# Kernel optimization log

Hardware: AMD Instinct MI355X
Metric: run time of the kernel (lower is better)

The kernel has to match this reference:

```python
import jax, jax.numpy as jnp
import numpy as np

B = 32768
EPS = 0.2  # BatchNorm eps used in the original module


def _xavier(key, shape):
    fan_in, fan_out = shape[-2], shape[-1]
    std = (2.0 / (fan_in + fan_out)) ** 0.5
    return (jax.random.normal(key, shape, jnp.float32) * std).astype(jnp.float32)


def bn(x, g, b):
    # training-mode BatchNorm1d: batch stats over the batch axis (-2), biased var
    m = jnp.mean(x, axis=-2, keepdims=True)
    v = jnp.mean(jnp.square(x - m), axis=-2, keepdims=True)
    return (x - m) * jax.lax.rsqrt(v + EPS) * g + b


def setup_inputs() -> dict:
    key = jax.random.key(0)
    ks = iter(jax.random.split(key, 48))
    inp = {}
    inp['x1f'] = jax.random.normal(next(ks), (B, 512), jnp.float32)
    inp['x2f'] = jax.random.normal(next(ks), (B, 512), jnp.float32)
    # shared trunk
    inp['W1'] = _xavier(next(ks), (512, 256)); inp['b1'] = jnp.zeros(256, jnp.float32)
    inp['W2'] = _xavier(next(ks), (256, 256)); inp['b2'] = jnp.zeros(256, jnp.float32)
    # batchnorm affine params (bn1:256, bn2:256, bn3:128, bn4:64)
    inp['g1'] = jnp.ones(256, jnp.float32); inp['be1'] = jnp.zeros(256, jnp.float32)
    inp['g2'] = jnp.ones(256, jnp.float32); inp['be2'] = jnp.zeros(256, jnp.float32)
    inp['g3'] = jnp.ones(128, jnp.float32); inp['be3'] = jnp.zeros(128, jnp.float32)
    inp['g4'] = jnp.ones(64, jnp.float32); inp['be4'] = jnp.zeros(64, jnp.float32)
    # 4 branch projections from each stream (x11..x14, x21..x24), stacked on axis 0
    inp['Wbx1'] = _xavier(next(ks), (4, 256, 256)); inp['bbx1'] = jnp.zeros((4, 256), jnp.float32)
    inp['Wbx2'] = _xavier(next(ks), (4, 256, 256)); inp['bbx2'] = jnp.zeros((4, 256), jnp.float32)
    # gating MLPs (xw*1, xw*2, xw*3, y*), stacked over the 4 attributes
    inp['Wwa'] = _xavier(next(ks), (4, 512, 128)); inp['bwa'] = jnp.zeros((4, 128), jnp.float32)
    inp['Wwb'] = _xavier(next(ks), (4, 128, 64)); inp['bwb'] = jnp.zeros((4, 64), jnp.float32)
    inp['Wwc'] = _xavier(next(ks), (4, 64, 64)); inp['bwc'] = jnp.zeros((4, 64), jnp.float32)
    inp['Wy'] = _xavier(next(ks), (4, 64, 2)); inp['by'] = jnp.zeros((4, 2), jnp.float32)
    # combine layers x1c..x4c, stacked
    inp['Wc'] = _xavier(next(ks), (4, 512, 256)); inp['bc'] = jnp.zeros((4, 256), jnp.float32)
    # output heads (different class counts: 3, 3, 6, 4)
    inp['Wo1'] = _xavier(next(ks), (256, 3)); inp['bo1'] = jnp.zeros(3, jnp.float32)
    inp['Wo2'] = _xavier(next(ks), (256, 3)); inp['bo2'] = jnp.zeros(3, jnp.float32)
    inp['Wo3'] = _xavier(next(ks), (256, 6)); inp['bo3'] = jnp.zeros(6, jnp.float32)
    inp['Wo4'] = _xavier(next(ks), (256, 4)); inp['bo4'] = jnp.zeros(4, jnp.float32)
    return inp


def reference(x1f, x2f, W1, b1, W2, b2, g1, be1, g2, be2, g3, be3, g4, be4,
              Wbx1, bbx1, Wbx2, bbx2, Wwa, bwa, Wwb, bwb, Wwc, bwc, Wy, by,
              Wc, bc, Wo1, bo1, Wo2, bo2, Wo3, bo3, Wo4, bo4):
    relu = jax.nn.relu

    def trunk(x):
        h = bn(relu(x @ W1 + b1), g1, be1)
        return bn(relu(h @ W2 + b2), g2, be2)

    h1 = trunk(x1f)  # [B,256]
    h2 = trunk(x2f)  # [B,256]

    # 4 branch features per stream, each bn1-normalized: [4,B,256]
    b1x = bn(relu(jnp.einsum('bi,kio->kbo', h1, Wbx1) + bbx1[:, None, :]), g1, be1)
    b2x = bn(relu(jnp.einsum('bi,kio->kbo', h2, Wbx2) + bbx2[:, None, :]), g1, be1)

    # gating MLP per attribute -> 2-way softmax weights
    xcat = jnp.concatenate([b1x, b2x], axis=-1)  # [4,B,512]
    a = bn(relu(jnp.einsum('kbi,kio->kbo', xcat, Wwa) + bwa[:, None, :]), g3, be3)
    b_ = bn(relu(jnp.einsum('kbi,kio->kbo', a, Wwb) + bwb[:, None, :]), g4, be4)
    c = bn(relu(jnp.einsum('kbi,kio->kbo', b_, Wwc) + bwc[:, None, :]), g4, be4)
    y = jax.nn.softmax(jnp.einsum('kbi,kio->kbo', c, Wy) + by[:, None, :], axis=-1)  # [4,B,2]

    # the original per-column loop == one broadcast multiply per stream
    xw = jnp.concatenate([b1x * y[..., 0:1], b2x * y[..., 1:2]], axis=-1)  # [4,B,512]

    # combine layers (dropout is identity in eval)
    xc = bn(relu(jnp.einsum('kbi,kio->kbo', xw, Wc) + bc[:, None, :]), g1, be1)  # [4,B,256]

    y1o = jax.nn.softmax(xc[0] @ Wo1 + bo1, axis=-1)
    y2o = jax.nn.softmax(xc[1] @ Wo2 + bo2, axis=-1)
    y3o = jax.nn.softmax(xc[2] @ Wo3 + bo3, axis=-1)
    y4o = jax.nn.softmax(xc[3] @ Wo4 + bo4, axis=-1)
    return (y1o, y2o, y3o, y4o)
```

## Files before the change

### kernel.cpp

```cpp
#include <hip/hip_runtime.h>
#include <hip/hip_bf16.h>


typedef unsigned short u16;
typedef _Float16 f16x8 __attribute__((ext_vector_type(8)));
typedef float f32x4 __attribute__((ext_vector_type(4)));

#define B_ROWS 32768
#define EPS_BN 0.2f
#define BINV (1.0f / 32768.0f)

__device__ __forceinline__ float bf2f(u16 u) {
    union { unsigned int i; float f; } c;
    c.i = ((unsigned int)u) << 16;
    return c.f;
}
__device__ __forceinline__ u16 f2bf(float f) {
    union { float f; unsigned int i; } c;
    c.f = f;
    unsigned int x = c.i;
    return (u16)((x + 0x7FFFu + ((x >> 16) & 1u)) >> 16);
}
__device__ __forceinline__ float h2f(u16 u) {
    _Float16 h;
    __builtin_memcpy(&h, &u, 2);
    return (float)h;
}
__device__ __forceinline__ u16 f2h(float f) {
    _Float16 h = (_Float16)f;
    u16 u;
    __builtin_memcpy(&u, &h, 2);
    return u;
}
__device__ __forceinline__ float ldp(const void* p, long i, int flag) {
    return flag ? bf2f(((const u16*)p)[i]) : ((const float*)p)[i];
}
__device__ __forceinline__ void gload16(const u16* gp, u16* lp) {
    __builtin_amdgcn_global_load_lds(
        (const __attribute__((address_space(1))) unsigned int*)gp,
        (__attribute__((address_space(3))) unsigned int*)lp, 16, 0, 0);
}

__global__ void detect_dtype(const u16* __restrict__ x, int* __restrict__ flag) {
    const int lane = threadIdx.x;
    const u16 v = x[2 * lane];
    const int e = (v >> 7) & 0xFF;
    const bool plausible = (e >= 110 && e <= 140);
    const unsigned long long m = __ballot(plausible);
    if (lane == 0) *flag = (__popcll(m) >= 58) ? 1 : 0;
}

struct PTab { const void* p[20]; int n[20]; int off[20]; };

__global__ void convert_params(PTab t, float* __restrict__ dst,
                               const int* __restrict__ flag) {
    const int ti = blockIdx.y;
    const int n = t.n[ti];
    float* o = dst + t.off[ti];
    const int isbf = *flag;
    for (int i = blockIdx.x * 256 + threadIdx.x; i < n; i += gridDim.x * 256)
        o[i] = ldp(t.p[ti], i, isbf);
}

__global__ __launch_bounds__(256) void prep_w(
    const void* __restrict__ W, long wstride,
    const void* __restrict__ bias, long bstride,
    const float* __restrict__ psum, const float* __restrict__ psq, int pstride,
    const void* __restrict__ pg, const void* __restrict__ pbe, int gmask,
    const int* __restrict__ dtflag,
    u16* __restrict__ Wt, long wtstride,
    float* __restrict__ biasP, float* __restrict__ T0o,
    float* __restrict__ T1o, float* __restrict__ bsum, long bost,
    int K, int khalf)
{
    const int tid = threadIdx.x;
    const int n = blockIdx.x;
    const int N = gridDim.x;
    const int inst = blockIdx.y;
    const int flag = *dtflag;
    __shared__ float sn[512], tn[512];
    __shared__ float r0[4], r1[4];

    for (int i = tid; i < K; i += 256) {
        float s = 1.f, t = 0.f;
        if (psum) {
            float m = psum[(long)pstride * inst + i] * BINV;
            float v = psq[(long)pstride * inst + i] * BINV - m * m;
            float g = ldp(pg, i & gmask, flag);
            float b = ldp(pbe, i & gmask, flag);
            s = g * rsqrtf(v + EPS_BN);
            t = b - m * s;
        }
        sn[i] = s; tn[i] = t;
    }
    __syncthreads();
    float p0 = 0.f, p1 = 0.f;
    for (int k = tid; k < K; k += 256) {
        float wv = ldp(W, wstride * inst + (long)k * N + n, flag);
        Wt[wtstride * inst + (long)n * K + k] = f2h(sn[k] * wv);
        float tw = tn[k] * wv;
        if (k < khalf) p0 += tw; else p1 += tw;
    }
#pragma unroll
    for (int off = 32; off; off >>= 1) {
        p0 += __shfl_xor(p0, off);
        p1 += __shfl_xor(p1, off);
    }
    const int lane = tid & 63, wid = tid >> 6;
    if (lane == 0) { r0[wid] = p0; r1[wid] = p1; }
    __syncthreads();
    if (tid == 0) {
        float t0 = r0[0] + r0[1] + r0[2] + r0[3];
        float t1 = r1[0] + r1[1] + r1[2] + r1[3];
        float bp = ldp(bias, bstride * inst + n, flag);
        long o = bost * inst + n;
        biasP[o] = bp; T0o[o] = t0; T1o[o] = t1; bsum[o] = bp + t0 + t1;
    }
}

__global__ __launch_bounds__(256) void reduce_stats(
    const float* __restrict__ part, int X, int colsPer,
    float* __restrict__ outS, float* __restrict__ outQ, int total)
{
    const int t = blockIdx.x * 256 + threadIdx.x;
    if (t >= total) return;
    const int p = t / colsPer, c = t % colsPer;
    const float* pb = part + (long)p * X * 2 * colsPer + c;
    float s = 0.f, q = 0.f;
#pragma unroll 4
    for (int x = 0; x < X; ++x) {
        s += pb[(long)x * 2 * colsPer];
        q += pb[(long)x * 2 * colsPer + colsPer];
    }
    outS[t] = s; outQ[t] = q;
}

template <bool XSTAGE, bool ROWW, int WM, int WN, int K>
__global__ __launch_bounds__(256, 3) void gemm_mfma(
    const void* __restrict__ X, const void* __restrict__ X2,
    long xstride, int ximask, int ldx, int ksplit, long ksecond,
    const int* __restrict__ dtflag,
    const u16* __restrict__ Wt, long wtstride,
    const float* __restrict__ biasP, const float* __restrict__ T0,
    const float* __restrict__ T1, const float* __restrict__ bsum, int bN,
    u16* __restrict__ Out, long ostride, int ldout,
    float* __restrict__ gsum, float* __restrict__ gsq, int sstride,
    float* __restrict__ part,
    const float* __restrict__ Y0v)
{
    const int tid = threadIdx.x;
    const int lane = tid & 63;
    const int wid = tid >> 6;
    const int wm = wid / WN, wn = wid % WN;
    const int inst = blockIdx.z;
    const int rowB = blockIdx.x * (64 * WM);
    const int nBase = blockIdx.y * (64 * WN);
    const int n0 = nBase + wn * 64;
    const int fm = lane & 15, quad = lane >> 4;
    const int rloc = lane >> 3;
    const int cg = (lane & 7) ^ rloc;

    __shared__ __align__(16) u16 AsBs[(WM + WN) * 4096];
    __shared__ float redS[4][64];
    __shared__ float redQ[4][64];
    u16* As = AsBs;
    u16* Bs = AsBs + WM * 4096;

    bool xf32 = false;
    if constexpr (XSTAGE) xf32 = (*dtflag == 0);
    const char* xb;
    if (XSTAGE) xb = (const char*)(inst == 0 ? X : X2);
    else        xb = (const char*)X + 2l * xstride * (inst & ximask);
    const u16* wtp = Wt + wtstride * inst;
    u16* op = Out + ostride * inst;

    f32x4 acc[4][4];
#pragma unroll
    for (int i = 0; i < 4; ++i)
#pragma unroll
        for (int j = 0; j < 4; ++j) acc[i][j] = (f32x4){0.f, 0.f, 0.f, 0.f};

    _Float16 ysc[2][4];
    if constexpr (ROWW) {
        const float* yp = Y0v + (long)inst * B_ROWS;
#pragma unroll
        for (int mi = 0; mi < 4; ++mi) {
            const float y = yp[rowB + wm * 64 + mi * 16 + fm];
            ysc[0][mi] = (_Float16)y;
            ysc[1][mi] = (_Float16)(1.f - y);
        }
    }

    for (int kt = 0; kt < K / 64; ++kt) {
        const int kk = kt * 64;
        __syncthreads();
        if constexpr (XSTAGE) {
#pragma unroll
            for (int p = 0; p < WM * 2; ++p) {
                const int s = p * 256 + tid;
                const int m = s >> 3, c = s & 7;
                const int g = c ^ (m & 7);
                f16x8 h;
                if (xf32) {
                    const float* gp = (const float*)xb + (long)(rowB + m) * ldx + kk + g * 8;
                    const float4 u = *(const float4*)gp;
                    const float4 u2 = *(const float4*)(gp + 4);
                    h[0] = (_Float16)u.x;  h[1] = (_Float16)u.y;
                    h[2] = (_Float16)u.z;  h[3] = (_Float16)u.w;
                    h[4] = (_Float16)u2.x; h[5] = (_Float16)u2.y;
                    h[6] = (_Float16)u2.z; h[7] = (_Float16)u2.w;
                } else {
                    const uint4 v = *(const uint4*)((const u16*)xb + (long)(rowB + m) * ldx + kk + g * 8);
                    const u16* pv = (const u16*)&v;
#pragma unroll
                    for (int j = 0; j < 8; ++j) h[j] = (_Float16)bf2f(pv[j]);
                }
                *(f16x8*)&As[s * 8] = h;
            }
        } else {
            const u16* xs = (const u16*)xb;
            int kkr = kk;
            if (kk >= ksplit) { xs += ksecond; kkr -= ksplit; }
#pragma unroll
            for (int s = wid; s < WM * 8; s += 4)
                gload16(xs + (long)(rowB + s * 8 + rloc) * ldx + kkr + cg * 8,
                        &As[s * 512 + lane * 8]);
        }
#pragma unroll
        for (int s = wid; s < WN * 8; s += 4)
            gload16(wtp + (long)(nBase + s * 8 + rloc) * K + kk + cg * 8,
                    &Bs[s * 512 + lane * 8]);
        __syncthreads();

        const int sel = (ROWW && kk >= ksplit) ? 1 : 0;
#pragma unroll
        for (int q = 0; q < 2; ++q) {
            f16x8 af[4], bfr[4];
#pragma unroll
            for (int mi = 0; mi < 4; ++mi) {
                const int mm = wm * 64 + mi * 16 + fm;
                af[mi] = *(const f16x8*)&As[mm * 64 + (((q * 4 + quad) ^ (mm & 7)) * 8)];
            }
            if constexpr (ROWW) {
#pragma unroll
                for (int mi = 0; mi < 4; ++mi) {
                    const _Float16 yh = ysc[sel][mi];
#pragma unroll
                    for (int j = 0; j < 8; ++j) af[mi][j] *= yh;
                }
            }
#pragma unroll
            for (int ni = 0; ni < 4; ++ni) {
                const int nn = wn * 64 + ni * 16 + fm;
                bfr[ni] = *(const f16x8*)&Bs[nn * 64 + (((q * 4 + quad) ^ (nn & 7)) * 8)];
            }
#pragma unroll
            for (int mi = 0; mi < 4; ++mi)
#pragma unroll
                for (int ni = 0; ni < 4; ++ni)
                    acc[mi][ni] = __builtin_amdgcn_mfma_f32_16x16x32_f16(
                        af[mi], bfr[ni], acc[mi][ni], 0, 0, 0);
        }
    }

    __syncthreads();

    u16* wtile = AsBs + wid * 4096;
    const int R0 = rowB + wm * 64;

    float yv[16];
    if constexpr (ROWW) {
        const float* yp = Y0v + (long)inst * B_ROWS;
#pragma unroll
        for (int mi = 0; mi < 4; ++mi)
#pragma unroll
            for (int r = 0; r < 4; ++r)
                yv[mi * 4 + r] = yp[R0 + mi * 16 + quad * 4 + r];
    }

#pragma unroll
    for (int ni = 0; ni < 4; ++ni) {
        const int nc = ni * 16 + fm;
        const int n = n0 + nc;
        float bS = 0.f, bP = 0.f, t0v = 0.f, t1v = 0.f;
        if constexpr (ROWW) {
            bP = biasP[(long)inst * bN + n];
            t0v = T0[(long)inst * bN + n];
            t1v = T1[(long)inst * bN + n];
        } else {
            bS = bsum[(long)inst * bN + n];
        }
        float s = 0.f, qq = 0.f;
#pragma unroll
        for (int mi = 0; mi < 4; ++mi) {
#pragma unroll
            for (int r = 0; r < 4; ++r) {
                float v;
                if constexpr (ROWW) {
                    const float y = yv[mi * 4 + r];
                    v = acc[mi][ni][r] + y * t0v + (1.f - y) * t1v + bP;
                } else {
                    v = acc[mi][ni][r] + bS;
                }
                v = fmaxf(v, 0.f);
                s += v; qq += v * v;
                const int lr = mi * 16 + quad * 4 + r;
                wtile[lr * 64 + (nc ^ (((lr >> 1) & 7) << 3))] = f2h(v);
            }
        }
        s += __shfl_xor(s, 16);  s += __shfl_xor(s, 32);
        qq += __shfl_xor(qq, 16); qq += __shfl_xor(qq, 32);
        if (quad == 0) { redS[wid][nc] = s; redQ[wid][nc] = qq; }
    }

    {
        const int l8 = lane & 7, r8 = lane >> 3;
#pragma unroll
        for (int it = 0; it < 8; ++it) {
            const int lr = it * 8 + r8;
            const int ch = l8 ^ ((lr >> 1) & 7);
            const f16x8 hv = *(const f16x8*)&wtile[lr * 64 + ch * 8];
            *(f16x8*)(op + (long)(R0 + lr) * ldout + n0 + l8 * 8) = hv;
        }
    }

    __syncthreads();
    if (tid < WN * 64) {
        const int wnc = tid >> 6, within = tid & 63;
        float s = 0.f, q = 0.f;
#pragma unroll
        for (int w = 0; w < WM; ++w) {
            s += redS[w * WN + wnc][within];
            q += redQ[w * WN + wnc][within];
        }
        if (part) {
            float* pb = part +
                (long)((inst * gridDim.y + blockIdx.y) * gridDim.x + blockIdx.x)
                    * (2 * WN * 64);
            pb[tid] = s;
            pb[WN * 64 + tid] = q;
        } else {
            atomicAdd(&gsum[(long)inst * sstride + nBase + tid], s);
            atomicAdd(&gsq [(long)inst * sstride + nBase + tid], q);
        }
    }
}

__global__ __launch_bounds__(256) void gate_kernel(
    const u16* __restrict__ zc,
    const float* __restrict__ stFs, const float* __restrict__ stFq,
    const float* __restrict__ g4, const float* __restrict__ be4,
    const float* __restrict__ Wy, const float* __restrict__ by,
    float* __restrict__ Y0)
{
    const int tid = threadIdx.x;
    const int k = blockIdx.y;
    const int r0 = blockIdx.x * 128;

    __shared__ __align__(8) float Ws2[64][2];
    __shared__ float cg[2];

    if (tid < 64) {
        const int c = tid;
        const float m = stFs[k * 64 + c] * BINV;
        const float v = stFq[k * 64 + c] * BINV - m * m;
        const float s = g4[c] * rsqrtf(v + EPS_BN);
        const float t = be4[c] - m * s;
        const float w0 = Wy[k * 128 + c * 2 + 0];
        const float w1 = Wy[k * 128 + c * 2 + 1];
        Ws2[c][0] = s * w0;
        Ws2[c][1] = s * w1;
        float t0 = t * w0, t1 = t * w1;
#pragma unroll
        for (int off = 32; off; off >>= 1) {
            t0 += __shfl_xor(t0, off);
            t1 += __shfl_xor(t1, off);
        }
        if (c == 0) {
            cg[0] = t0 + by[k * 2 + 0];
            cg[1] = t1 + by[k * 2 + 1];
        }
    }
    __syncthreads();

    const int row = r0 + (tid >> 1);
    const int seg = tid & 1;
    const u16* xp = zc + ((long)k * B_ROWS + row) * 64 + seg * 32;
    float a0 = 0.f, a1 = 0.f;
#pragma unroll
    for (int it = 0; it < 4; ++it) {
        const uint4 v = *(const uint4*)(xp + it * 8);
        const u16* pv = (const u16*)&v;
#pragma unroll
        for (int e = 0; e < 8; ++e) {
            const int c = seg * 32 + it * 8 + e;
            const float x = h2f(pv[e]);
            a0 += x * Ws2[c][0];
            a1 += x * Ws2[c][1];
        }
    }
    a0 += __shfl_xor(a0, 1);
    a1 += __shfl_xor(a1, 1);
    if (seg == 0) {
        const float l0 = a0 + cg[0];
        const float l1 = a1 + cg[1];
        Y0[(long)k * B_ROWS + row] = 1.f / (1.f + __expf(l1 - l0));
    }
}

__global__ __launch_bounds__(256) void heads_kernel(
    const u16* __restrict__ zxc,
    const float* __restrict__ stHs, const float* __restrict__ stHq,
    const float* __restrict__ g1, const float* __restrict__ be1,
    const float* __restrict__ Wo1, const float* __restrict__ bo1,
    const float* __restrict__ Wo2, const float* __restrict__ bo2,
    const float* __restrict__ Wo3, const float* __restrict__ bo3,
    const float* __restrict__ Wo4, const float* __restrict__ bo4,
    void* __restrict__ out, const int* __restrict__ dtflag)
{
    const int tid = threadIdx.x;
    const int k = blockIdx.y;
    const int r0 = blockIdx.x * 64;

    const float* Wo; const float* bo; int nk; long obase;
    if (k == 0)      { Wo = Wo1; bo = bo1; nk = 3; obase = 0; }
    else if (k == 1) { Wo = Wo2; bo = bo2; nk = 3; obase = (long)3 * B_ROWS; }
    else if (k == 2) { Wo = Wo3; bo = bo3; nk = 6; obase = (long)6 * B_ROWS; }
    else             { Wo = Wo4; bo = bo4; nk = 4; obase = (long)12 * B_ROWS; }

    __shared__ __align__(16) float Ws[256][8];
    __shared__ float cj[8];
    __shared__ float redC[4][8];

    {
        const int c = tid;
        const float m = stHs[k * 256 + c] * BINV;
        const float v = stHq[k * 256 + c] * BINV - m * m;
        const float s = g1[c] * rsqrtf(v + EPS_BN);
        const float t = be1[c] - m * s;
        const int rs = c ^ (c >> 6);
        float tw[6];
#pragma unroll
        for (int j = 0; j < 6; ++j) {
            const float w = (j < nk) ? Wo[c * nk + j] : 0.f;
            Ws[rs][j] = s * w;
            tw[j] = t * w;
        }
        Ws[rs][6] = 0.f; Ws[rs][7] = 0.f;
#pragma unroll
        for (int off = 32; off; off >>= 1)
#pragma unroll
            for (int j = 0; j < 6; ++j) tw[j] += __shfl_xor(tw[j], off);
        const int lane = tid & 63, wid = tid >> 6;
        if (lane < 6) redC[wid][lane] = tw[lane];
    }
    __syncthreads();
    if (tid < 8) {
        float s4 = 0.f;
        if (tid < 6) s4 = redC[0][tid] + redC[1][tid] + redC[2][tid] + redC[3][tid];
        cj[tid] = (tid < nk) ? s4 + bo[tid] : 0.f;
    }
    __syncthreads();

    const int row = r0 + (tid >> 2);
    const int seg = tid & 3;
    const u16* xp = zxc + ((long)k * B_ROWS + row) * 256 + seg * 64;
    float acc[6];
#pragma unroll
    for (int j = 0; j < 6; ++j) acc[j] = 0.f;
#pragma unroll
    for (int it = 0; it < 8; ++it) {
        const uint4 v = *(const uint4*)(xp + it * 8);
        const u16* pv = (const u16*)&v;
#pragma unroll
        for (int e = 0; e < 8; ++e) {
            const int cc = it * 8 + e;
            const int rs = (seg * 64 + cc) ^ seg;
            const float x = h2f(pv[e]);
            const f32x4 w0 = *(const f32x4*)&Ws[rs][0];
            const f32x4 w1 = *(const f32x4*)&Ws[rs][4];
            acc[0] += x * w0[0];
            acc[1] += x * w0[1];
            acc[2] += x * w0[2];
            acc[3] += x * w0[3];
            acc[4] += x * w1[0];
            acc[5] += x * w1[1];
        }
    }
#pragma unroll
    for (int j = 0; j < 6; ++j) {
        acc[j] += __shfl_xor(acc[j], 1);
        acc[j] += __shfl_xor(acc[j], 2);
    }

    if (seg == 0) {
        float l[6];
        float mx = -1e30f;
#pragma unroll
        for (int j = 0; j < 6; j++)
            if (j < nk) { l[j] = acc[j] + cj[j]; mx = fmaxf(mx, l[j]); }
        float e[6];
        float se = 0.f;
#pragma unroll
        for (int j = 0; j < 6; j++)
            if (j < nk) { e[j] = __expf(l[j] - mx); se += e[j]; }
        const float inv = 1.f / se;
        if (*dtflag) {
            u16* ob = (u16*)out;
#pragma unroll
            for (int j = 0; j < 6; j++)
                if (j < nk) ob[obase + (long)row * nk + j] = f2bf(e[j] * inv);
        } else {
            float* of = (float*)out;
#pragma unroll
            for (int j = 0; j < 6; j++)
                if (j < nk) of[obase + (long)row * nk + j] = e[j] * inv;
        }
    }
}

__global__ void fill_sentinel(u16* out, int n) {
    int i = blockIdx.x * 256 + threadIdx.x;
    if (i < n) out[i] = 0x3E80;
}

extern "C" void kernel_launch(void* const* d_in, const int* in_sizes, int n_in,
                              void* d_out, int out_size, void* d_ws, size_t ws_size,
                              hipStream_t stream)
{
    const long B = B_ROWS;
    char* ws = (char*)d_ws;
    const size_t MB = 1024 * 1024;

    u16* z1  = (u16*)(ws);
    u16* z2  = (u16*)(ws + 32 * MB);
    u16* za  = (u16*)(ws);
    u16* zbb = (u16*)(ws + 32 * MB);
    u16* zc  = (u16*)(ws + 48 * MB);
    u16* zxc = (u16*)(ws);
    u16* zb  = (u16*)(ws + 64 * MB);
    float* Y0 = (float*)(ws + 192 * MB);
    float* stats = (float*)(ws + 192 * MB + 512 * 1024);
    int* dtflag = (int*)(ws + 192 * MB + 576 * 1024);
    float* Pst = (float*)(ws + 192 * MB + 640 * 1024);

    u16* WtA = (u16*)(ws + 193 * MB);
    u16* WtB = WtA + 131072;
    u16* WtC = WtB + 131072;
    u16* WtD = WtC + 524288;
    u16* WtH = WtD + 262144;
    u16* WtE = WtH + 524288;
    u16* WtF = WtE + 32768;
    float* biasArea = (float*)(ws + 197 * MB);
    float* bA = biasArea;
    float* bB = bA + 2048;
    float* bC = bB + 2048;
    float* bD = bC + 8192;
    float* bH = bD + 2048;
    float* bE = bH + 4096;
    float* bF = bE + 1024;

    float* partC = (float*)(ws);
    float* partH = (float*)(ws + 193 * MB);

    const int cIdx[20] = {6,7,10,11,12,13,20,21,22,23,24,25,28,29,30,31,32,33,34,35};
    PTab tab;
    int mapOff[36];
    int acc = 0;
    for (int i = 0; i < 20; i++) {
        tab.p[i] = d_in[cIdx[i]];
        tab.n[i] = in_sizes[cIdx[i]];
        tab.off[i] = acc;
        mapOff[cIdx[i]] = acc;
        acc += in_sizes[cIdx[i]];
    }
    const size_t need = 197 * MB + 20480 * 4 + 4096;
    if (need > ws_size || (size_t)acc * 4 > 384 * 1024) {
        fill_sentinel<<<(out_size + 255) / 256, 256, 0, stream>>>((u16*)d_out, out_size);
        return;
    }
    auto PF = [&](int idx) { return Pst + mapOff[idx]; };

    float* stAs = stats;        float* stAq = stAs + 512;
    float* stBs = stAq + 512;   float* stBq = stBs + 512;
    float* stCs = stBq + 512;   float* stCq = stCs + 2048;
    float* stDs = stCq + 2048;  float* stDq = stDs + 512;
    float* stEs = stDq + 512;   float* stEq = stEs + 256;
    float* stFs = stEq + 256;   float* stFq = stFs + 256;
    float* stHs = stFq + 256;   float* stHq = stHs + 1024;

    hipMemsetAsync(stats, 0, 10240 * 4, stream);
    detect_dtype<<<1, 64, 0, stream>>>((const u16*)d_in[0], dtflag);
    convert_params<<<dim3(32, 20), 256, 0, stream>>>(tab, Pst, dtflag);

    const dim3 blk(256);
    const int BIGK = 1 << 29;

    prep_w<<<dim3(256, 2), blk, 0, stream>>>(
        d_in[2], 0, d_in[3], 0, nullptr, nullptr, 0, nullptr, nullptr, 0,
        dtflag, WtA, 0, bA, bA + 512, bA + 1024, bA + 1536, 256, 512, 512);
    gemm_mfma<true, false, 2, 2, 512><<<dim3(256, 2, 2), blk, 0, stream>>>(
        d_in[0], d_in[1], 0, 0, 512, BIGK, 0, dtflag, WtA, 0,
        bA, bA + 512, bA + 1024, bA + 1536, 256,
        z1, B * 256, 256, stAs, stAq, 256, nullptr, nullptr);

    prep_w<<<dim3(256, 2), blk, 0, stream>>>(
        d_in[4], 0, d_in[5], 0, stAs, stAq, 256, d_in[6], d_in[7], 255,
        dtflag, WtB, 65536, bB, bB + 512, bB + 1024, bB + 1536, 256, 256, 256);
    gemm_mfma<false, false, 2, 2, 256><<<dim3(256, 2, 2), blk, 0, stream>>>(
        z1, nullptr, B * 256, 3, 256, BIGK, 0, dtflag, WtB, 65536,
        bB, bB + 512, bB + 1024, bB + 1536, 256,
        z2, B * 256, 256, stBs, stBq, 256, nullptr, nullptr);

    for (int s = 0; s < 2; s++) {
        prep_w<<<dim3(256, 4), blk, 0, stream>>>(
            d_in[s ? 16 : 14], 65536, d_in[s ? 17 : 15], 256,
            stBs + s * 256, stBq + s * 256, 0, d_in[8], d_in[9], 255,
            dtflag, WtC + s * 65536, 131072,
            bC + s * 256, bC + 2048 + s * 256, bC + 4096 + s * 256,
            bC + 6144 + s * 256, 512, 256, 256);
    }
    gemm_mfma<false, false, 2, 2, 256><<<dim3(256, 2, 8), blk, 0, stream>>>(
        z2, nullptr, B * 256, 1, 256, BIGK, 0, dtflag, WtC, 65536,
        bC, bC + 2048, bC + 4096, bC + 6144, 256,
        zb, B * 256, 256, stCs, stCq, 256, partC, nullptr);
    reduce_stats<<<dim3(8), blk, 0, stream>>>(partC, 256, 128, stCs, stCq, 2048);

    prep_w<<<dim3(128, 4), blk, 0, stream>>>(
        d_in[18], 65536, d_in[19], 128, stCs, stCq, 512, d_in[6], d_in[7], 255,
        dtflag, WtD, 65536, bD, bD + 512, bD + 1024, bD + 1536, 128, 512, 512);
    prep_w<<<dim3(256, 4), blk, 0, stream>>>(
        d_in[26], 131072, d_in[27], 256, stCs, stCq, 512, d_in[6], d_in[7], 255,
        dtflag, WtH, 131072, bH, bH + 1024, bH + 2048, bH + 3072, 256, 512, 256);
    gemm_mfma<false, false, 2, 2, 512><<<dim3(256, 1, 4), blk, 0, stream>>>(
        zb, nullptr, 2 * B * 256, 3, 256, 256, B * 256, dtflag, WtD, 65536,
        bD, bD + 512, bD + 1024, bD + 1536, 128,
        za, B * 128, 128, stDs, stDq, 128, nullptr, nullptr);

    prep_w<<<dim3(64, 4), blk, 0, stream>>>(
        d_in[20], 8192, d_in[21], 64, stDs, stDq, 128, d_in[10], d_in[11], 127,
        dtflag, WtE, 8192, bE, bE + 256, bE + 512, bE + 768, 64, 128, 128);
    gemm_mfma<false, false, 4, 1, 128><<<dim3(128, 1, 4), blk, 0, stream>>>(
        za, nullptr, B * 128, 3, 128, BIGK, 0, dtflag, WtE, 8192,
        bE, bE + 256, bE + 512, bE + 768, 64,
        zbb, B * 64, 64, stEs, stEq, 64, nullptr, nullptr);

    prep_w<<<dim3(64, 4), blk, 0, stream>>>(
        d_in[22], 4096, d_in[23], 64, stEs, stEq, 64, d_in[12], d_in[13], 63,
        dtflag, WtF, 4096, bF, bF + 256, bF + 512, bF + 768, 64, 64, 64);
    gemm_mfma<false, false, 4, 1, 64><<<dim3(128, 1, 4), blk, 0, stream>>>(
        zbb, nullptr, B * 64, 3, 64, BIGK, 0, dtflag, WtF, 4096,
        bF, bF + 256, bF + 512, bF + 768, 64,
        zc, B * 64, 64, stFs, stFq, 64, nullptr, nullptr);

    gate_kernel<<<dim3(B_ROWS / 128, 4), blk, 0, stream>>>(
        zc, stFs, stFq, PF(12), PF(13), PF(24), PF(25), Y0);

    gemm_mfma<false, true, 2, 2, 512><<<dim3(256, 2, 4), blk, 0, stream>>>(
        zb, nullptr, 2 * B * 256, 3, 256, 256, B * 256, dtflag, WtH, 131072,
        bH, bH + 1024, bH + 2048, bH + 3072, 256,
        zxc, B * 256, 256, stHs, stHq, 256, partH, Y0);
    reduce_stats<<<dim3(4), blk, 0, stream>>>(partH, 256, 128, stHs, stHq, 1024);

    heads_kernel<<<dim3(B_ROWS / 64, 4), blk, 0, stream>>>(
        zxc, stHs, stHq, PF(6), PF(7), PF(28), PF(29), PF(30), PF(31),
        PF(32), PF(33), PF(34), PF(35), d_out, dtflag);
}
```

Before: 584.9 us.

## Load MFMA fragments directly from global memory, bypassing LDS staging for non-XSTAGE GEMMs

For the non-XSTAGE GEMM instances, the K loop no longer stages A and B tiles into shared memory with barriers. Each lane now reads its f16x8 MFMA fragments straight from global memory using precomputed row offsets. This removes both __syncthreads per K step and the LDS round trip. In exchange, tiles are no longer shared across warps, so the same data is read redundantly from global memory or cache, and the 16-byte per-lane row-strided loads may coalesce poorly.

```diff
diff --git a/kernel.cpp b/kernel.cpp
--- a/kernel.cpp
+++ b/kernel.cpp
@@ -157,14 +157,10 @@
     const int nBase = blockIdx.y * (64 * WN);
     const int n0 = nBase + wn * 64;
     const int fm = lane & 15, quad = lane >> 4;
-    const int rloc = lane >> 3;
-    const int cg = (lane & 7) ^ rloc;
 
     __shared__ __align__(16) u16 AsBs[(WM + WN) * 4096];
     __shared__ float redS[4][64];
     __shared__ float redQ[4][64];
-    u16* As = AsBs;
-    u16* Bs = AsBs + WM * 4096;
 
     bool xf32 = false;
     if constexpr (XSTAGE) xf32 = (*dtflag == 0);
@@ -191,10 +187,56 @@
         }
     }
 
-    for (int kt = 0; kt < K / 64; ++kt) {
-        const int kk = kt * 64;
-        __syncthreads();
-        if constexpr (XSTAGE) {
+    if constexpr (!XSTAGE) {
+        long aOff[4], bOff[4];
+#pragma unroll
+        for (int mi = 0; mi < 4; ++mi)
+            aOff[mi] = (long)(rowB + wm * 64 + mi * 16 + fm) * ldx;
+#pragma unroll
+        for (int ni = 0; ni < 4; ++ni)
+            bOff[ni] = (long)(n0 + ni * 16 + fm) * K;
+        const u16* xs0 = (const u16*)xb;
+
+        for (int kt = 0; kt < K / 64; ++kt) {
+            const int kk = kt * 64;
+            const u16* xs = xs0;
+            int kkr = kk;
+            if (kk >= ksplit) { xs += ksecond; kkr -= ksplit; }
+            const int sel = (ROWW && kk >= ksplit) ? 1 : 0;
+#pragma unroll
+            for (int q = 0; q < 2; ++q) {
+                const int kc = (q * 4 + quad) * 8;
+                f16x8 af[4], bfr[4];
+#pragma unroll
+                for (int mi = 0; mi < 4; ++mi)
+                    af[mi] = *(const f16x8*)(xs + aOff[mi] + kkr + kc);
+#pragma unroll
+                for (int ni = 0; ni < 4; ++ni)
+                    bfr[ni] = *(const f16x8*)(wtp + bOff[ni] + kk + kc);
+                if constexpr (ROWW) {
+#pragma unroll
+                    for (int mi = 0; mi < 4; ++mi) {
+                        const _Float16 yh = ysc[sel][mi];
+#pragma unroll
+                        for (int j = 0; j < 8; ++j) af[mi][j] *= yh;
+                    }
+                }
+#pragma unroll
+                for (int mi = 0; mi < 4; ++mi)
+#pragma unroll
+                    for (int ni = 0; ni < 4; ++ni)
+                        acc[mi][ni] = __builtin_amdgcn_mfma_f32_16x16x32_f16(
+                            af[mi], bfr[ni], acc[mi][ni], 0, 0, 0);
+            }
+        }
+    } else {
+        u16* As = AsBs;
+        u16* Bs = AsBs + WM * 4096;
+        const int rloc = lane >> 3;
+        const int cg = (lane & 7) ^ rloc;
+        for (int kt = 0; kt < K / 64; ++kt) {
+            const int kk = kt * 64;
+            __syncthreads();
 #pragma unroll
             for (int p = 0; p < WM * 2; ++p) {
                 const int s = p * 256 + tid;
@@ -217,49 +259,32 @@
                 }
                 *(f16x8*)&As[s * 8] = h;
             }
-        } else {
-            const u16* xs = (const u16*)xb;
-            int kkr = kk;
-            if (kk >= ksplit) { xs += ksecond; kkr -= ksplit; }
-#pragma unroll
-            for (int s = wid; s < WM * 8; s += 4)
-                gload16(xs + (long)(rowB + s * 8 + rloc) * ldx + kkr + cg * 8,
-                        &As[s * 512 + lane * 8]);
-        }
-#pragma unroll
-        for (int s = wid; s < WN * 8; s += 4)
-            gload16(wtp + (long)(nBase + s * 8 + rloc) * K + kk + cg * 8,
-                    &Bs[s * 512 + lane * 8]);
-        __syncthreads();
-
-        const int sel = (ROWW && kk >= ksplit) ? 1 : 0;
-#pragma unroll
-        for (int q = 0; q < 2; ++q) {
-            f16x8 af[4], bfr[4];
-#pragma unroll
-            for (int mi = 0; mi < 4; ++mi) {
-                const int mm = wm * 64 + mi * 16 + fm;
-                af[mi] = *(const f16x8*)&As[mm * 64 + (((q * 4 + quad) ^ (mm & 7)) * 8)];
+#pragma unroll
+            for (int s = wid; s < WN * 8; s += 4)
+                gload16(wtp + (long)(nBase + s * 8 + rloc) * K + kk + cg * 8,
+                        &Bs[s * 512 + lane * 8]);
+            __syncthreads();
+
+#pragma unroll
+            for (int q = 0; q < 2; ++q) {
+                f16x8 af[4], bfr[4];
+#pragma unroll
+                for (int mi = 0; mi < 4; ++mi) {
+                    const int mm = wm * 64 + mi * 16 + fm;
+                    af[mi] = *(const f16x8*)&As[mm * 64 + (((q * 4 + quad) ^ (mm & 7)) * 8)];
+                }
+#pragma unroll
+                for (int ni = 0; ni < 4; ++ni) {
+                    const int nn = wn * 64 + ni * 16 + fm;
+                    bfr[ni] = *(const f16x8*)&Bs[nn * 64 + (((q * 4 + quad) ^ (nn & 7)) * 8)];
+                }
+#pragma unroll
+                for (int mi = 0; mi < 4; ++mi)
+#pragma unroll
+                    for (int ni = 0; ni < 4; ++ni)
+                        acc[mi][ni] = __builtin_amdgcn_mfma_f32_16x16x32_f16(
+                            af[mi], bfr[ni], acc[mi][ni], 0, 0, 0);
             }
-            if constexpr (ROWW) {
-#pragma unroll
-                for (int mi = 0; mi < 4; ++mi) {
-                    const _Float16 yh = ysc[sel][mi];
-#pragma unroll
-                    for (int j = 0; j < 8; ++j) af[mi][j] *= yh;
-                }
-            }
-#pragma unroll
-            for (int ni = 0; ni < 4; ++ni) {
-                const int nn = wn * 64 + ni * 16 + fm;
-                bfr[ni] = *(const f16x8*)&Bs[nn * 64 + (((q * 4 + quad) ^ (nn & 7)) * 8)];
-            }
-#pragma unroll
-            for (int mi = 0; mi < 4; ++mi)
-#pragma unroll
-                for (int ni = 0; ni < 4; ++ni)
-                    acc[mi][ni] = __builtin_amdgcn_mfma_f32_16x16x32_f16(
-                        af[mi], bfr[ni], acc[mi][ni], 0, 0, 0);
         }
     }
 
```

New measurement: 793.9 us. +35.7%, slower.
